# Kernel optimization log

Hardware: AMD Instinct MI355X
Metric: run time of the kernel (lower is better)

## Reference

```python
import jax, jax.numpy as jnp
import numpy as np

B, N, F, D, H = 4, 2048, 128, 128, 4

def setup_inputs() -> dict:
    key = jax.random.key(0)
    k1, k2, k3, k4 = jax.random.split(key, 4)
    X = jax.random.normal(k1, (B, N, F), dtype=jnp.float32)
    A = jax.random.uniform(k2, (B, N, N), dtype=jnp.float32)
    kernel = jax.random.normal(k3, (F, D), dtype=jnp.float32) * 0.05
    bias = jnp.ones((D,), dtype=jnp.float32)
    attn = jax.random.normal(k4, (H, D, D), dtype=jnp.float32) * 0.05
    return {"X": X, "A": A, "kernel": kernel, "bias": bias, "attn": attn}

def reference(X, A, kernel, bias, attn):
    # Linear projection: [B,N,F] @ [F,D] + bias -> [B,N,D]
    Xp = jnp.einsum('bnf,fd->bnd', X, kernel) + bias
    # Per-head bilinear scores Xp @ attn_h @ Xp^T, batched over heads: [B,H,N,N]
    scores = jnp.einsum('bnd,hde,bme->bhnm', Xp, attn, Xp)
    # Adjacency mask + tanh (fused elementwise)
    Am = jnp.tanh(A[:, None, :, :] * scores)
    # Weighted aggregate per head: [B,H,N,N] @ [B,N,D] -> [B,H,N,D]
    heads = jnp.einsum('bhnm,bmd->bhnd', Am, Xp)
    # Mean over heads, relu
    Xh = jax.nn.relu(jnp.mean(heads, axis=1))
    # Skip connection (shapes match since F == D): relu(Xh + X)
    out = jax.nn.relu(Xh + X)
    return out
```

## Files before the change

kernel.cpp:

```cpp
#include <hip/hip_runtime.h>

#define NB 4
#define NN 2048
#define ND 128
#define NH 4

typedef short short8 __attribute__((ext_vector_type(8)));
typedef short short4v __attribute__((ext_vector_type(4)));
typedef float floatx4 __attribute__((ext_vector_type(4)));

__device__ __forceinline__ short f2bf(float f){
  unsigned u = __float_as_uint(f);
  u += 0x7FFFu + ((u >> 16) & 1u);
  return (short)(u >> 16);
}
__device__ __forceinline__ float bf2f(short s){
  unsigned u = ((unsigned)(unsigned short)s) << 16;
  return __uint_as_float(u);
}

__global__ void k0_transpose(const float* __restrict__ W, const float* __restrict__ attn,
                             short* __restrict__ WT, short* __restrict__ attnT){
  int mat = blockIdx.x;
  const float* src = (mat == 0) ? W : (attn + (mat - 1) * 16384);
  short* dst = (mat == 0) ? WT : (attnT + (mat - 1) * 16384);
  __shared__ short tile[128 * 130];
  int t = threadIdx.x;
  for (int k = 0; k < 64; ++k){
    int idx = k * 256 + t;
    int r = idx >> 7, c = idx & 127;
    tile[c * 130 + r] = f2bf(src[idx]);
  }
  __syncthreads();
  for (int k = 0; k < 8; ++k){
    int g = k * 256 + t;
    int r = g >> 4, c8 = g & 15;
    short8 v;
    #pragma unroll
    for (int j = 0; j < 8; ++j) v[j] = tile[r * 130 + c8 * 8 + j];
    *(short8*)&dst[r * 128 + c8 * 8] = v;
  }
}

__global__ __launch_bounds__(256) void k1_xp(const float* __restrict__ X,
                                             const short* __restrict__ WT,
                                             const float* __restrict__ bias,
                                             short* __restrict__ Xp){
  int bid = blockIdx.x;
  int b = bid >> 5, i0 = (bid & 31) << 6;
  int t = threadIdx.x, w = t >> 6, lane = t & 63, lq = lane >> 4, lc = lane & 15;
  __shared__ __align__(16) short ldsB[16384];
  #pragma unroll
  for (int c = 0; c < 8; ++c){
    int q = c * 256 + t; int fblk = q >> 7; int d = q & 127;
    *(short8*)&ldsB[q * 8] = *(const short8*)&WT[d * 128 + fblk * 8];
  }
  short8 af[4][4];
  #pragma unroll
  for (int ib = 0; ib < 4; ++ib)
    #pragma unroll
    for (int k = 0; k < 4; ++k){
      const float* xp = &X[(b * NN + i0 + ib * 16 + lc) * ND + k * 32 + lq * 8];
      float4 x0 = *(const float4*)xp;
      float4 x1 = *(const float4*)(xp + 4);
      short8 s;
      s[0]=f2bf(x0.x); s[1]=f2bf(x0.y); s[2]=f2bf(x0.z); s[3]=f2bf(x0.w);
      s[4]=f2bf(x1.x); s[5]=f2bf(x1.y); s[6]=f2bf(x1.z); s[7]=f2bf(x1.w);
      af[ib][k] = s;
    }
  __syncthreads();
  floatx4 acc[4][2];
  #pragma unroll
  for (int ib = 0; ib < 4; ++ib)
    #pragma unroll
    for (int eb = 0; eb < 2; ++eb) acc[ib][eb] = (floatx4){0.f, 0.f, 0.f, 0.f};
  #pragma unroll
  for (int eb = 0; eb < 2; ++eb)
    #pragma unroll
    for (int k = 0; k < 4; ++k){
      short8 bf = *(short8*)&ldsB[(k * 4 + lq) * 1024 + (w * 32 + eb * 16 + lc) * 8];
      #pragma unroll
      for (int ib = 0; ib < 4; ++ib)
        acc[ib][eb] = __builtin_amdgcn_mfma_f32_16x16x32_bf16(af[ib][k], bf, acc[ib][eb], 0, 0, 0);
    }
  #pragma unroll
  for (int ib = 0; ib < 4; ++ib)
    #pragma unroll
    for (int eb = 0; eb < 2; ++eb){
      int d = w * 32 + eb * 16 + lc;
      float bv = bias[d];
      #pragma unroll
      for (int r = 0; r < 4; ++r){
        int n = i0 + ib * 16 + lq * 4 + r;
        Xp[(b * NN + n) * ND + d] = f2bf(acc[ib][eb][r] + bv);
      }
    }
}

__global__ void k1b_transpose(const short* __restrict__ Xp, short* __restrict__ XpT){
  int bid = blockIdx.x;
  int b = bid >> 6; int rem = bid & 63;
  int n0 = (rem >> 1) << 6, d0 = (rem & 1) << 6;
  __shared__ short tile[64 * 66];
  int t = threadIdx.x;
  #pragma unroll
  for (int c = 0; c < 2; ++c){
    int g = c * 256 + t; int r = g >> 3, c8 = g & 7;
    short8 v = *(const short8*)&Xp[(b * NN + n0 + r) * ND + d0 + c8 * 8];
    #pragma unroll
    for (int j = 0; j < 8; ++j) tile[(c8 * 8 + j) * 66 + r] = v[j];
  }
  __syncthreads();
  #pragma unroll
  for (int c = 0; c < 2; ++c){
    int g = c * 256 + t; int d = g >> 3, n8 = g & 7;
    short8 v;
    #pragma unroll
    for (int j = 0; j < 8; ++j) v[j] = tile[d * 66 + n8 * 8 + j];
    *(short8*)&XpT[(b * ND + d0 + d) * NN + n0 + n8 * 8] = v;
  }
}

__global__ __launch_bounds__(256) void k2_y(const short* __restrict__ Xp,
                                            const short* __restrict__ attnT,
                                            short* __restrict__ Y){
  int bid = blockIdx.x;
  int it = bid & 31, h = (bid >> 5) & 3, b = bid >> 7;
  int i0 = it << 6;
  int t = threadIdx.x, w = t >> 6, lane = t & 63, lq = lane >> 4, lc = lane & 15;
  __shared__ __align__(16) short ldsB[16384];
  const short* Bsrc = attnT + h * 16384;
  #pragma unroll
  for (int c = 0; c < 8; ++c){
    int q = c * 256 + t; int dblk = q >> 7; int e = q & 127;
    *(short8*)&ldsB[q * 8] = *(const short8*)&Bsrc[e * 128 + dblk * 8];
  }
  short8 af[4][4];
  #pragma unroll
  for (int ib = 0; ib < 4; ++ib)
    #pragma unroll
    for (int k = 0; k < 4; ++k)
      af[ib][k] = *(const short8*)&Xp[(b * NN + i0 + ib * 16 + lc) * ND + k * 32 + lq * 8];
  __syncthreads();
  floatx4 acc[4][2];
  #pragma unroll
  for (int ib = 0; ib < 4; ++ib)
    #pragma unroll
    for (int eb = 0; eb < 2; ++eb) acc[ib][eb] = (floatx4){0.f, 0.f, 0.f, 0.f};
  #pragma unroll
  for (int eb = 0; eb < 2; ++eb)
    #pragma unroll
    for (int k = 0; k < 4; ++k){
      short8 bf = *(short8*)&ldsB[(k * 4 + lq) * 1024 + (w * 32 + eb * 16 + lc) * 8];
      #pragma unroll
      for (int ib = 0; ib < 4; ++ib)
        acc[ib][eb] = __builtin_amdgcn_mfma_f32_16x16x32_bf16(af[ib][k], bf, acc[ib][eb], 0, 0, 0);
    }
  #pragma unroll
  for (int ib = 0; ib < 4; ++ib)
    #pragma unroll
    for (int eb = 0; eb < 2; ++eb){
      int e = w * 32 + eb * 16 + lc;
      #pragma unroll
      for (int r = 0; r < 4; ++r){
        int n = i0 + ib * 16 + lq * 4 + r;
        Y[((b * NH + h) * NN + n) * ND + e] = f2bf(acc[ib][eb][r]);
      }
    }
}

__global__ __launch_bounds__(256, 3) void k3_fused(const short* __restrict__ Xp,
                                                   const short* __restrict__ XpT,
                                                   const short* __restrict__ Y,
                                                   const float* __restrict__ A,
                                                   float* __restrict__ part){
  int bid = blockIdx.x;
  int it = bid & 127, b = (bid >> 7) & 3, ms = bid >> 9;
  int i0 = it << 4;
  int t = threadIdx.x, w = t >> 6, lane = t & 63, lq = lane >> 4, lc = lane & 15;

  __shared__ __align__(16) short ldsXpT[2][8320];
  __shared__ __align__(16) short ldsPh[2][1024];
  __shared__ __align__(16) short ldsPl[2][1024];

  short8 yf[4][4];
  #pragma unroll
  for (int h = 0; h < 4; ++h)
    #pragma unroll
    for (int k = 0; k < 4; ++k)
      yf[h][k] = *(const short8*)&Y[((b * NH + h) * NN + i0 + lc) * ND + k * 32 + lq * 8];

  floatx4 acc[2];
  acc[0] = (floatx4){0.f,0.f,0.f,0.f};
  acc[1] = (floatx4){0.f,0.f,0.f,0.f};

  const int mbase = ms << 9;
  const int poff = (w * 2 + (lq >> 1)) * 128 + lc * 8 + (lq & 1) * 4;

  for (int itn = 0; itn < 8; ++itn){
    int p = itn & 1;
    int m0 = mbase + itn * 64;
    const short* src = XpT + b * (ND * NN) + m0;
    #pragma unroll
    for (int c = 0; c < 4; ++c){
      int q = c * 256 + t; int d = q >> 3, mb = q & 7;
      *(short8*)&ldsXpT[p][mb * 1040 + d * 8] = *(const short8*)&src[d * NN + mb * 8];
    }
    short8 xpf[4];
    const short* xr = Xp + (b * NN + m0 + w * 16 + lc) * ND;
    #pragma unroll
    for (int k = 0; k < 4; ++k) xpf[k] = *(const short8*)&xr[k * 32 + lq * 8];
    floatx4 av = *(const floatx4*)&A[(b * NN + i0 + lc) * NN + m0 + w * 16 + lq * 4];

    float psum[4] = {0.f, 0.f, 0.f, 0.f};
    #pragma unroll
    for (int h = 0; h < 4; ++h){
      floatx4 S = (floatx4){0.f,0.f,0.f,0.f};
      #pragma unroll
      for (int k = 0; k < 4; ++k)
        S = __builtin_amdgcn_mfma_f32_16x16x32_bf16(xpf[k], yf[h][k], S, 0, 0, 0);
      #pragma unroll
      for (int r = 0; r < 4; ++r){
        float x = av[r] * S[r];
        float e = __builtin_amdgcn_exp2f(x * 2.885390081777926f);
        psum[r] += 1.f - 2.f * __builtin_amdgcn_rcpf(e + 1.f);
      }
    }
    short4v hi4, lo4;
    #pragma unroll
    for (int r = 0; r < 4; ++r){
      float pb = 0.25f * psum[r];
      short h16 = f2bf(pb);
      hi4[r] = h16;
      lo4[r] = f2bf(pb - bf2f(h16));
    }
    *(short4v*)&ldsPh[p][poff] = hi4;
    *(short4v*)&ldsPl[p][poff] = lo4;
    __syncthreads();

    #pragma unroll
    for (int kb = 0; kb < 2; ++kb){
      short8 ph = *(short8*)&ldsPh[p][(kb * 4 + lq) * 128 + lc * 8];
      short8 pl = *(short8*)&ldsPl[p][(kb * 4 + lq) * 128 + lc * 8];
      #pragma unroll
      for (int db = 0; db < 2; ++db){
        short8 bfr = *(short8*)&ldsXpT[p][(kb * 4 + lq) * 1040 + (w * 32 + db * 16 + lc) * 8];
        acc[db] = __builtin_amdgcn_mfma_f32_16x16x32_bf16(ph, bfr, acc[db], 0, 0, 0);
        acc[db] = __builtin_amdgcn_mfma_f32_16x16x32_bf16(pl, bfr, acc[db], 0, 0, 0);
      }
    }
  }
  float* dst = part + (size_t)ms * 1048576 + (b * NN + i0) * ND;
  #pragma unroll
  for (int db = 0; db < 2; ++db)
    #pragma unroll
    for (int r = 0; r < 4; ++r)
      dst[(lq * 4 + r) * ND + w * 32 + db * 16 + lc] = acc[db][r];
}

__global__ void k4_final(const float* __restrict__ part, const float* __restrict__ X,
                         float* __restrict__ out){
  int f = (blockIdx.x * 256 + threadIdx.x) * 4;
  float4 s0 = *(const float4*)(part + f);
  float4 s1 = *(const float4*)(part + 1048576 + f);
  float4 s2 = *(const float4*)(part + 2097152 + f);
  float4 s3 = *(const float4*)(part + 3145728 + f);
  float4 xv = *(const float4*)(X + f);
  float4 o;
  o.x = fmaxf(fmaxf(s0.x + s1.x + s2.x + s3.x, 0.f) + xv.x, 0.f);
  o.y = fmaxf(fmaxf(s0.y + s1.y + s2.y + s3.y, 0.f) + xv.y, 0.f);
  o.z = fmaxf(fmaxf(s0.z + s1.z + s2.z + s3.z, 0.f) + xv.z, 0.f);
  o.w = fmaxf(fmaxf(s0.w + s1.w + s2.w + s3.w, 0.f) + xv.w, 0.f);
  *(float4*)(out + f) = o;
}

extern "C" void kernel_launch(void* const* d_in, const int* in_sizes, int n_in,
                              void* d_out, int out_size, void* d_ws, size_t ws_size,
                              hipStream_t stream) {
  const float* X    = (const float*)d_in[0];
  const float* A    = (const float*)d_in[1];
  const float* W    = (const float*)d_in[2];
  const float* bias = (const float*)d_in[3];
  const float* attn = (const float*)d_in[4];
  float* out = (float*)d_out;

  const size_t OFF_XP    = 0;
  const size_t OFF_XPT   = (size_t)2 << 20;
  const size_t OFF_Y     = (size_t)4 << 20;
  const size_t OFF_PART  = (size_t)12 << 20;
  const size_t OFF_WT    = (size_t)28 << 20;
  const size_t OFF_ATTNT = OFF_WT + 32768;
  const size_t NEED = OFF_ATTNT + 131072;
  if (ws_size < NEED) return;

  char* ws = (char*)d_ws;
  short* Xp    = (short*)(ws + OFF_XP);
  short* XpT   = (short*)(ws + OFF_XPT);
  short* Y     = (short*)(ws + OFF_Y);
  float* part  = (float*)(ws + OFF_PART);
  short* WT    = (short*)(ws + OFF_WT);
  short* attnT = (short*)(ws + OFF_ATTNT);

  k0_transpose<<<5, 256, 0, stream>>>(W, attn, WT, attnT);
  k1_xp<<<128, 256, 0, stream>>>(X, WT, bias, Xp);
  k1b_transpose<<<256, 256, 0, stream>>>(Xp, XpT);
  k2_y<<<512, 256, 0, stream>>>(Xp, attnT, Y);
  k3_fused<<<2048, 256, 0, stream>>>(Xp, XpT, Y, A, part);
  k4_final<<<1024, 256, 0, stream>>>(part, X, out);
}
```

Before: 185.6 us.

## Load PV B-operand directly from global and prefetch next Xp/A tiles

Drops the shared-memory staging of the transposed Xp tile and has each wave load its MFMA B fragments for the aggregation step straight from global memory. The next iteration's Xp fragments and adjacency values are software-prefetched into registers before the barrier. The tanh accumulation is algebraically simplified so only the reciprocal sum is kept and the 1 - 0.5*sum combine happens once. The barrier becomes a raw waitcnt plus s_barrier. This cuts LDS traffic and barrier stalls but adds register pressure and issues strided, less coalesced global loads for the B operand.

```diff
diff --git a/kernel.cpp b/kernel.cpp
--- a/kernel.cpp
+++ b/kernel.cpp
@@ -179,7 +179,6 @@
   int i0 = it << 4;
   int t = threadIdx.x, w = t >> 6, lane = t & 63, lq = lane >> 4, lc = lane & 15;
 
-  __shared__ __align__(16) short ldsXpT[2][8320];
   __shared__ __align__(16) short ldsPh[2][1024];
   __shared__ __align__(16) short ldsPl[2][1024];
 
@@ -197,46 +196,60 @@
   const int mbase = ms << 9;
   const int poff = (w * 2 + (lq >> 1)) * 128 + lc * 8 + (lq & 1) * 4;
 
+  const short* xr  = Xp  + (size_t)(b * NN + mbase + w * 16 + lc) * ND;
+  const short* pvB = XpT + (size_t)(b * ND + w * 32 + lc) * NN + mbase;
+  const float* Ar  = A   + (size_t)(b * NN + i0 + lc) * NN + mbase + w * 16 + lq * 4;
+
+  short8 xpf_c[4];
+  #pragma unroll
+  for (int k = 0; k < 4; ++k) xpf_c[k] = *(const short8*)&xr[k * 32 + lq * 8];
+  floatx4 av_c = *(const floatx4*)Ar;
+
   for (int itn = 0; itn < 8; ++itn){
     int p = itn & 1;
-    int m0 = mbase + itn * 64;
-    const short* src = XpT + b * (ND * NN) + m0;
-    #pragma unroll
-    for (int c = 0; c < 4; ++c){
-      int q = c * 256 + t; int d = q >> 3, mb = q & 7;
-      *(short8*)&ldsXpT[p][mb * 1040 + d * 8] = *(const short8*)&src[d * NN + mb * 8];
-    }
-    short8 xpf[4];
-    const short* xr = Xp + (b * NN + m0 + w * 16 + lc) * ND;
-    #pragma unroll
-    for (int k = 0; k < 4; ++k) xpf[k] = *(const short8*)&xr[k * 32 + lq * 8];
-    floatx4 av = *(const floatx4*)&A[(b * NN + i0 + lc) * NN + m0 + w * 16 + lq * 4];
-
-    float psum[4] = {0.f, 0.f, 0.f, 0.f};
+    short8 pvb[2][2];
+    #pragma unroll
+    for (int kb = 0; kb < 2; ++kb)
+      #pragma unroll
+      for (int db = 0; db < 2; ++db)
+        pvb[kb][db] = *(const short8*)&pvB[(size_t)(db * 16) * NN + kb * 32 + lq * 8];
+
+    float av2[4];
+    #pragma unroll
+    for (int r = 0; r < 4; ++r) av2[r] = av_c[r] * 2.885390081777926f;
+    float rs[4] = {0.f, 0.f, 0.f, 0.f};
     #pragma unroll
     for (int h = 0; h < 4; ++h){
       floatx4 S = (floatx4){0.f,0.f,0.f,0.f};
       #pragma unroll
       for (int k = 0; k < 4; ++k)
-        S = __builtin_amdgcn_mfma_f32_16x16x32_bf16(xpf[k], yf[h][k], S, 0, 0, 0);
+        S = __builtin_amdgcn_mfma_f32_16x16x32_bf16(xpf_c[k], yf[h][k], S, 0, 0, 0);
       #pragma unroll
       for (int r = 0; r < 4; ++r){
-        float x = av[r] * S[r];
-        float e = __builtin_amdgcn_exp2f(x * 2.885390081777926f);
-        psum[r] += 1.f - 2.f * __builtin_amdgcn_rcpf(e + 1.f);
+        float e = __builtin_amdgcn_exp2f(av2[r] * S[r]);
+        rs[r] += __builtin_amdgcn_rcpf(e + 1.f);
       }
     }
+
+    int adv = (itn < 7) ? 64 : 0;
+    xr += (size_t)adv * ND; Ar += adv; 
+    short8 xpf_n[4];
+    #pragma unroll
+    for (int k = 0; k < 4; ++k) xpf_n[k] = *(const short8*)&xr[k * 32 + lq * 8];
+    floatx4 av_n = *(const floatx4*)Ar;
+
     short4v hi4, lo4;
     #pragma unroll
     for (int r = 0; r < 4; ++r){
-      float pb = 0.25f * psum[r];
+      float pb = 1.f - 0.5f * rs[r];
       short h16 = f2bf(pb);
       hi4[r] = h16;
       lo4[r] = f2bf(pb - bf2f(h16));
     }
     *(short4v*)&ldsPh[p][poff] = hi4;
     *(short4v*)&ldsPl[p][poff] = lo4;
-    __syncthreads();
+
+    asm volatile("s_waitcnt lgkmcnt(0)\n\ts_barrier" ::: "memory");
 
     #pragma unroll
     for (int kb = 0; kb < 2; ++kb){
@@ -244,11 +257,14 @@
       short8 pl = *(short8*)&ldsPl[p][(kb * 4 + lq) * 128 + lc * 8];
       #pragma unroll
       for (int db = 0; db < 2; ++db){
-        short8 bfr = *(short8*)&ldsXpT[p][(kb * 4 + lq) * 1040 + (w * 32 + db * 16 + lc) * 8];
-        acc[db] = __builtin_amdgcn_mfma_f32_16x16x32_bf16(ph, bfr, acc[db], 0, 0, 0);
-        acc[db] = __builtin_amdgcn_mfma_f32_16x16x32_bf16(pl, bfr, acc[db], 0, 0, 0);
+        acc[db] = __builtin_amdgcn_mfma_f32_16x16x32_bf16(ph, pvb[kb][db], acc[db], 0, 0, 0);
+        acc[db] = __builtin_amdgcn_mfma_f32_16x16x32_bf16(pl, pvb[kb][db], acc[db], 0, 0, 0);
       }
     }
+    pvB += adv;
+    #pragma unroll
+    for (int k = 0; k < 4; ++k) xpf_c[k] = xpf_n[k];
+    av_c = av_n;
   }
   float* dst = part + (size_t)ms * 1048576 + (b * NN + i0) * ND;
   #pragma unroll
```

Result: slower. 196.5 us (+5.9%).
